# Optimization experiments

Measured on AMD Instinct MI355X. Metric: run time of the kernel, lower is better.

Reference implementation:

```python
import jax, jax.numpy as jnp
import numpy as np
from jax import lax

DN = ('NCHW', 'OIHW', 'NCHW')

def conv2d(x, w, b, pad):
    y = lax.conv_general_dilated(x, w, (1, 1), [(pad, pad), (pad, pad)], dimension_numbers=DN)
    return y + b[None, :, None, None]

def setup_inputs() -> dict:
    key = jax.random.key(0)
    ks = jax.random.split(key, 12)
    B, H, W, C, K = 32, 256, 256, 16, 32
    x = jax.random.normal(ks[0], (B, 1, H, W), jnp.float32)
    s = 0.1
    stem_w = jax.random.normal(ks[1], (C, 1, 3, 3), jnp.float32) * s
    stem_b = jnp.zeros((C,), jnp.float32)
    up1_w = jax.random.normal(ks[2], (C, C, 3, 3), jnp.float32) * s
    up1_b = jnp.zeros((C,), jnp.float32)
    up2_w = jax.random.normal(ks[3], (C, C, 1, 1), jnp.float32) * s
    up2_b = jnp.zeros((C,), jnp.float32)
    tau_w = jax.random.normal(ks[4], (C, C, 1, 1), jnp.float32) * s
    tau_b = jnp.zeros((C,), jnp.float32)
    codebook = jax.random.uniform(ks[5], (K, C), jnp.float32, -1.0 / K, 1.0 / K)
    dec_w = jax.random.normal(ks[6], (1, C, 1, 1), jnp.float32) * s
    dec_b = jnp.zeros((1,), jnp.float32)
    return {"x": x, "stem_w": stem_w, "stem_b": stem_b, "up1_w": up1_w, "up1_b": up1_b,
            "up2_w": up2_w, "up2_b": up2_b, "tau_w": tau_w, "tau_b": tau_b,
            "codebook": codebook, "dec_w": dec_w, "dec_b": dec_b, "n_steps": 5}

def vq(z, codebook):
    # z: [B,C,H,W], codebook: [K,C]
    B, C, H, W = z.shape
    K = codebook.shape[0]
    z_flat = jnp.transpose(z, (0, 2, 3, 1)).reshape(-1, C)  # [N,C]
    dists = (jnp.sum(z_flat ** 2, axis=1, keepdims=True)
             + jnp.sum(codebook ** 2, axis=1)
             - 2.0 * z_flat @ codebook.T)  # [N,K]
    indices = jnp.argmin(dists, axis=1)  # [N]
    z_q = jnp.transpose(codebook[indices].reshape(B, H, W, C), (0, 3, 1, 2))
    commit_loss = jnp.mean((lax.stop_gradient(z_q) - z) ** 2)
    codebook_loss = jnp.mean((z_q - lax.stop_gradient(z)) ** 2)
    vq_loss = codebook_loss + 0.25 * commit_loss
    z_q_st = z + lax.stop_gradient(z_q - z)
    used = jnp.zeros((K,), jnp.float32).at[indices].set(1.0)
    usage = jnp.sum(used) / K
    return z_q_st, vq_loss, usage, indices.reshape(B, H, W)

def reference(x, stem_w, stem_b, up1_w, up1_b, up2_w, up2_b, tau_w, tau_b, codebook, dec_w, dec_b, n_steps):
    state = jax.nn.relu(conv2d(x, stem_w, stem_b, 1))
    vq_total = jnp.float32(0.0)
    usage_total = jnp.float32(0.0)
    for _ in range(n_steps):
        delta = conv2d(jax.nn.relu(conv2d(state, up1_w, up1_b, 1)), up2_w, up2_b, 0)
        beta = jax.nn.sigmoid(conv2d(state, tau_w, tau_b, 0))
        state = beta * state + (1.0 - beta) * delta
        state, vq_loss, usage, _ = vq(state, codebook)
        vq_total = vq_total + vq_loss
        usage_total = usage_total + usage
    output = jax.nn.sigmoid(conv2d(state, dec_w, dec_b, 0))
    return output, vq_total / n_steps, usage_total / n_steps
```

## Files before the change

### kernel.cpp

```cpp
#include <hip/hip_runtime.h>
#include <math.h>

#define DEV __device__ __forceinline__

namespace {
constexpr int B_ = 32, H_ = 256, W_ = 256;
constexpr size_t NPIX = (size_t)B_ * H_ * W_;

constexpr int QT9 = 0;
constexpr int QAB = 5940;
constexpr int QCB = 7220;
constexpr int QU2 = 7860;
constexpr int QTOT = 8116;
constexpr int QLDS = 7220;

constexpr int IW1 = 0;
constexpr int IU2 = 2304;
constexpr int ITA = 2560;
constexpr int ICB = 2816;
constexpr int IB1 = 3456;
constexpr int IB2 = 3472;
constexpr int ITB = 3488;
constexpr int ISB = 3504;
constexpr int ISW = 3520;
constexpr int ITOT = 3664;

constexpr size_t OFF_QTAB = 2 * NPIX;
constexpr size_t OFF_ITAB = OFF_QTAB + (size_t)QTOT * 4;
constexpr size_t OFF_DLUT = OFF_ITAB + (size_t)ITOT * 4;
constexpr size_t OFF_LOSS = (OFF_DLUT + 128 + 7) & ~(size_t)7;
constexpr size_t OFF_MASK = OFF_LOSS + 5 * 8;
}

typedef float f2v __attribute__((ext_vector_type(2)));

struct V16 { f2v h[8]; };

DEV f2v fma2(f2v a, f2v b, f2v c) {
#if __has_builtin(__builtin_elementwise_fma)
    return __builtin_elementwise_fma(a, b, c);
#else
    f2v r; r.x = fmaf(a.x, b.x, c.x); r.y = fmaf(a.y, b.y, c.y); return r;
#endif
}
DEV f2v max2(f2v a, f2v b) {
#if __has_builtin(__builtin_elementwise_max)
    return __builtin_elementwise_max(a, b);
#else
    f2v r; r.x = fmaxf(a.x, b.x); r.y = fmaxf(a.y, b.y); return r;
#endif
}

DEV V16 v16z() {
    V16 r;
    #pragma unroll
    for (int j = 0; j < 8; ++j) r.h[j] = (f2v){0.f, 0.f};
    return r;
}
DEV void v16fma(V16& a, const V16& w, float s) {
    f2v ss = (f2v){s, s};
    #pragma unroll
    for (int j = 0; j < 8; ++j) a.h[j] = fma2(w.h[j], ss, a.h[j]);
}
DEV void v16add(V16& a, const V16& b) {
    #pragma unroll
    for (int j = 0; j < 8; ++j) a.h[j] = a.h[j] + b.h[j];
}
DEV void v16relu(V16& a) {
    f2v z = (f2v){0.f, 0.f};
    #pragma unroll
    for (int j = 0; j < 8; ++j) a.h[j] = max2(a.h[j], z);
}
DEV float v16dot(const V16& a, const V16& b) {
    f2v acc = (f2v){0.f, 0.f};
    #pragma unroll
    for (int j = 0; j < 8; ++j) acc = fma2(a.h[j], b.h[j], acc);
    return acc.x + acc.y;
}
DEV V16 ld16(const float* p) {
    const float4* q = (const float4*)p;
    float4 A = q[0], Bv = q[1], C = q[2], D = q[3];
    V16 r;
    r.h[0] = (f2v){A.x, A.y};  r.h[1] = (f2v){A.z, A.w};
    r.h[2] = (f2v){Bv.x, Bv.y}; r.h[3] = (f2v){Bv.z, Bv.w};
    r.h[4] = (f2v){C.x, C.y};  r.h[5] = (f2v){C.z, C.w};
    r.h[6] = (f2v){D.x, D.y};  r.h[7] = (f2v){D.z, D.w};
    return r;
}
DEV void st16(float* p, const V16& v) {
    float4* q = (float4*)p;
    q[0] = make_float4(v.h[0].x, v.h[0].y, v.h[1].x, v.h[1].y);
    q[1] = make_float4(v.h[2].x, v.h[2].y, v.h[3].x, v.h[3].y);
    q[2] = make_float4(v.h[4].x, v.h[4].y, v.h[5].x, v.h[5].y);
    q[3] = make_float4(v.h[6].x, v.h[6].y, v.h[7].x, v.h[7].y);
}
DEV void v16sig(V16& a) {
    #pragma unroll
    for (int j = 0; j < 8; ++j) {
        a.h[j].x = 1.f / (1.f + expf(-a.h[j].x));
        a.h[j].y = 1.f / (1.f + expf(-a.h[j].y));
    }
}

__global__ void k_setup(const float* __restrict__ w1, const float* __restrict__ b1,
                        const float* __restrict__ u2w, const float* __restrict__ b2,
                        const float* __restrict__ tw, const float* __restrict__ tb,
                        const float* __restrict__ cb, const float* __restrict__ stw,
                        const float* __restrict__ stb, const float* __restrict__ dw,
                        const float* __restrict__ db,
                        float* __restrict__ gQ, float* __restrict__ gI,
                        float* __restrict__ dlut, double* __restrict__ lossS,
                        unsigned int* __restrict__ maskS)
{
    int tid = threadIdx.x;
    if (tid < 5) { lossS[tid] = 0.0; maskS[tid] = 0u; }
    for (int e = tid; e < 297; e += 256) {
        int t = e / 33, k = e % 33;
        float* dst = &gQ[QT9 + e * 20];
        for (int o = 0; o < 16; ++o) {
            float acc = 0.f;
            if (k < 32) {
                for (int i = 0; i < 16; ++i)
                    acc = fmaf(w1[o * 144 + i * 9 + t], cb[k * 16 + i], acc);
                if (t == 4) acc += b1[o];
            }
            dst[o] = acc;
        }
        dst[16] = dst[17] = dst[18] = dst[19] = 0.f;
    }
    if (tid < 32) {
        int k = tid;
        float nrm = 0.f;
        for (int c = 0; c < 16; ++c) { float v = cb[k * 16 + c]; nrm = fmaf(v, v, nrm); }
        for (int c = 0; c < 16; ++c) { gQ[QCB + k * 20 + c] = cb[k * 16 + c]; gI[ICB + k * 20 + c] = cb[k * 16 + c]; }
        gQ[QCB + k * 20 + 16] = nrm; gI[ICB + k * 20 + 16] = nrm;
        for (int c = 17; c < 20; ++c) { gQ[QCB + k * 20 + c] = 0.f; gI[ICB + k * 20 + c] = 0.f; }
        float dacc = db[0];
        for (int c = 0; c < 16; ++c) dacc = fmaf(dw[c], cb[k * 16 + c], dacc);
        dlut[k] = 1.f / (1.f + expf(-dacc));
        for (int c = 0; c < 16; ++c) {
            float ta = tb[c];
            for (int i = 0; i < 16; ++i) ta = fmaf(tw[c * 16 + i], cb[k * 16 + i], ta);
            float beta = 1.f / (1.f + expf(-ta));
            gQ[QAB + k * 20 + c] = beta * cb[k * 16 + c] + (1.f - beta) * b2[c];
            gQ[QAB + (32 + k) * 20 + c] = 1.f - beta;
        }
        for (int c = 16; c < 20; ++c) { gQ[QAB + k * 20 + c] = 0.f; gQ[QAB + (32 + k) * 20 + c] = 0.f; }
    }
    if (tid < 16) {
        int i = tid;
        for (int o = 0; o < 16; ++o) {
            gQ[QU2 + i * 16 + o] = u2w[o * 16 + i];
            gI[IU2 + i * 16 + o] = u2w[o * 16 + i];
            gI[ITA + i * 16 + o] = tw[o * 16 + i];
        }
        gI[IB1 + i] = b1[i]; gI[IB2 + i] = b2[i]; gI[ITB + i] = tb[i]; gI[ISB + i] = stb[i];
    }
    for (int e = tid; e < 144; e += 256) {
        int t = e / 16, i = e % 16;
        float* dst = &gI[IW1 + e * 16];
        for (int o = 0; o < 16; ++o) dst[o] = w1[o * 144 + i * 9 + t];
    }
    if (tid < 9) {
        int t = tid;
        for (int o = 0; o < 16; ++o) gI[ISW + t * 16 + o] = stw[o * 9 + t];
    }
}

__global__ __launch_bounds__(256, 3) void k_iter1(
    const float* __restrict__ x, const float* __restrict__ gI,
    unsigned char* __restrict__ idx_out, double* __restrict__ lossS,
    unsigned int* __restrict__ maskS)
{
    __shared__ __align__(16) float xt[20 * 36];
    __shared__ __align__(16) float stE[306 * 20];
    __shared__ __align__(16) float stO[306 * 20];
    __shared__ double dsum[4];
    __shared__ unsigned int msum[4];
    const int lx = threadIdx.x, ly = threadIdx.y;
    const int lid = ly * 16 + lx;
    const int b = blockIdx.z, oy = blockIdx.y * 16, ox = blockIdx.x * 32;
    const float* xb = x + (size_t)b * (H_ * W_);
    for (int i = lid; i < 720; i += 256) {
        int iy = i / 36, ix = i % 36;
        int gy = oy - 2 + iy, gx = ox - 2 + ix;
        float v = 0.f;
        if ((unsigned)gy < (unsigned)H_ && (unsigned)gx < (unsigned)W_) v = xb[gy * W_ + gx];
        xt[i] = v;
    }
    __syncthreads();
    for (int q = lid; q < 612; q += 256) {
        int sy = q / 34, sx = q % 34;
        int gy = oy - 1 + sy, gx = ox - 1 + sx;
        bool inb = ((unsigned)gy < (unsigned)H_ && (unsigned)gx < (unsigned)W_);
        V16 a = ld16(&gI[ISB]);
        #pragma unroll
        for (int t = 0; t < 9; ++t) {
            float xv = xt[(sy + t / 3) * 36 + sx + t % 3];
            V16 w = ld16(&gI[ISW + t * 16]);
            v16fma(a, w, xv);
        }
        v16relu(a);
        if (!inb) a = v16z();
        float* dst = ((sx & 1) ? stO : stE) + (sy * 17 + (sx >> 1)) * 20;
        st16(dst, a);
    }
    __syncthreads();
    V16 u0 = ld16(&gI[IB1]);
    V16 u1 = u0;
    #pragma unroll
    for (int t = 0; t < 9; ++t) {
        const int r = ly + t / 3, dx = t % 3;
        const float* p0; const float* p1;
        if (dx == 0)      { p0 = &stE[(r * 17 + lx) * 20];     p1 = &stO[(r * 17 + lx) * 20]; }
        else if (dx == 1) { p0 = &stO[(r * 17 + lx) * 20];     p1 = &stE[(r * 17 + lx + 1) * 20]; }
        else              { p0 = &stE[(r * 17 + lx + 1) * 20]; p1 = &stO[(r * 17 + lx + 1) * 20]; }
        V16 s0 = ld16(p0), s1 = ld16(p1);
        const int base = IW1 + t * 256;
        #pragma unroll
        for (int j = 0; j < 8; ++j) {
            f2v a0 = s0.h[j], a1 = s1.h[j];
            V16 wA = ld16(&gI[base + (2 * j) * 16]);
            v16fma(u0, wA, a0.x); v16fma(u1, wA, a1.x);
            V16 wB = ld16(&gI[base + (2 * j + 1) * 16]);
            v16fma(u0, wB, a0.y); v16fma(u1, wB, a1.y);
        }
    }
    v16relu(u0); v16relu(u1);
    V16 c0 = ld16(&stO[((ly + 1) * 17 + lx) * 20]);
    V16 c1 = ld16(&stE[((ly + 1) * 17 + lx + 1) * 20]);
    V16 v0 = ld16(&gI[IB2]);
    V16 v1 = v0;
    #pragma unroll
    for (int j = 0; j < 8; ++j) {
        f2v a0 = u0.h[j], a1 = u1.h[j];
        V16 wA = ld16(&gI[IU2 + (2 * j) * 16]);
        v16fma(v0, wA, a0.x); v16fma(v1, wA, a1.x);
        V16 wB = ld16(&gI[IU2 + (2 * j + 1) * 16]);
        v16fma(v0, wB, a0.y); v16fma(v1, wB, a1.y);
    }
    V16 t0 = ld16(&gI[ITB]);
    V16 t1 = t0;
    #pragma unroll
    for (int j = 0; j < 8; ++j) {
        f2v a0 = c0.h[j], a1 = c1.h[j];
        V16 wA = ld16(&gI[ITA + (2 * j) * 16]);
        v16fma(t0, wA, a0.x); v16fma(t1, wA, a1.x);
        V16 wB = ld16(&gI[ITA + (2 * j + 1) * 16]);
        v16fma(t0, wB, a0.y); v16fma(t1, wB, a1.y);
    }
    v16sig(t0); v16sig(t1);
    V16 z0, z1;
    #pragma unroll
    for (int j = 0; j < 8; ++j) {
        z0.h[j] = fma2(t0.h[j], c0.h[j] - v0.h[j], v0.h[j]);
        z1.h[j] = fma2(t1.h[j], c1.h[j] - v1.h[j], v1.h[j]);
    }
    float zz0 = v16dot(z0, z0), zz1 = v16dot(z1, z1);
    float best0 = 3.4e38f, best1 = 3.4e38f; int bk0 = 0, bk1 = 0;
    #pragma unroll 4
    for (int k = 0; k < 32; ++k) {
        V16 q = ld16(&gI[ICB + k * 20]);
        float cn = gI[ICB + k * 20 + 16];
        float d0 = (zz0 + cn) - 2.0f * v16dot(q, z0);
        float d1 = (zz1 + cn) - 2.0f * v16dot(q, z1);
        if (d0 < best0) { best0 = d0; bk0 = k; }
        if (d1 < best1) { best1 = d1; bk1 = k; }
    }
    unsigned short pr = (unsigned short)(bk0 | (bk1 << 8));
    *(unsigned short*)(idx_out + (size_t)b * (H_ * W_) + (size_t)(oy + ly) * W_ + ox + 2 * lx) = pr;
    float lp = best0 + best1;
    unsigned int m = (1u << bk0) | (1u << bk1);
    #pragma unroll
    for (int off = 32; off > 0; off >>= 1) {
        lp += __shfl_down(lp, off, 64);
        m |= __shfl_down(m, off, 64);
    }
    if ((lid & 63) == 0) { dsum[lid >> 6] = (double)lp; msum[lid >> 6] = m; }
    __syncthreads();
    if (lid == 0) {
        atomicAdd(lossS, dsum[0] + dsum[1] + dsum[2] + dsum[3]);
        atomicOr(maskS, msum[0] | msum[1] | msum[2] | msum[3]);
    }
}

__global__ __launch_bounds__(256, 3) void k_qstep(
    const unsigned char* __restrict__ idx_in, unsigned char* __restrict__ idx_out,
    const float* __restrict__ gQ, double* __restrict__ lossS,
    unsigned int* __restrict__ maskS)
{
    __shared__ __align__(16) float tab[QLDS];
    __shared__ unsigned char ct[18 * 80];
    __shared__ double dsum[4];
    __shared__ unsigned int msum[4];
    const int tx = threadIdx.x, ty = threadIdx.y;
    const int lid = ty * 16 + tx;
    const int b = blockIdx.z, oy = blockIdx.y * 16, ox = blockIdx.x * 64;
    for (int i = lid; i < QLDS / 4; i += 256) ((float4*)tab)[i] = ((const float4*)gQ)[i];
    const unsigned char* ib = idx_in + (size_t)b * (H_ * W_);
    for (int i = lid; i < 18 * 66; i += 256) {
        int r = i / 66, c = i % 66;
        int gy = oy - 1 + r, gx = ox - 1 + c;
        unsigned char v = 32;
        if ((unsigned)gy < (unsigned)H_ && (unsigned)gx < (unsigned)W_) v = ib[gy * W_ + gx];
        ct[r * 80 + c] = v;
    }
    __syncthreads();
    const int cx = tx * 4;
    int K[3][6];
    #pragma unroll
    for (int r = 0; r < 3; ++r) {
        unsigned int w0 = *(const unsigned int*)&ct[(ty + r) * 80 + cx];
        unsigned int w1 = *(const unsigned int*)&ct[(ty + r) * 80 + cx + 4];
        K[r][0] = w0 & 255; K[r][1] = (w0 >> 8) & 255; K[r][2] = (w0 >> 16) & 255;
        K[r][3] = w0 >> 24; K[r][4] = w1 & 255; K[r][5] = (w1 >> 8) & 255;
    }
    V16 V[4];
    #pragma unroll
    for (int half = 0; half < 2; ++half) {
        V16 U0 = v16z(), U1 = v16z();
        const int p0 = half * 2, p1 = half * 2 + 1;
        #pragma unroll
        for (int t = 0; t < 9; ++t) {
            const int dy = t / 3, dx = t % 3;
            V16 e0 = ld16(&tab[(t * 33 + K[dy][p0 + dx]) * 20]);
            v16add(U0, e0);
            V16 e1 = ld16(&tab[(t * 33 + K[dy][p1 + dx]) * 20]);
            v16add(U1, e1);
        }
        v16relu(U0); v16relu(U1);
        V16 v0 = v16z(), v1 = v16z();
        #pragma unroll
        for (int j = 0; j < 8; ++j) {
            f2v a0 = U0.h[j], a1 = U1.h[j];
            V16 wA = ld16(&gQ[QU2 + (2 * j) * 16]);
            v16fma(v0, wA, a0.x); v16fma(v1, wA, a1.x);
            V16 wB = ld16(&gQ[QU2 + (2 * j + 1) * 16]);
            v16fma(v0, wB, a0.y); v16fma(v1, wB, a1.y);
        }
        {
            int kc = K[1][p0 + 1];
            V16 a = ld16(&tab[QAB + kc * 20]);
            V16 bb = ld16(&tab[QAB + (32 + kc) * 20]);
            #pragma unroll
            for (int j = 0; j < 8; ++j) v0.h[j] = fma2(bb.h[j], v0.h[j], a.h[j]);
        }
        {
            int kc = K[1][p1 + 1];
            V16 a = ld16(&tab[QAB + kc * 20]);
            V16 bb = ld16(&tab[QAB + (32 + kc) * 20]);
            #pragma unroll
            for (int j = 0; j < 8; ++j) v1.h[j] = fma2(bb.h[j], v1.h[j], a.h[j]);
        }
        V[p0] = v0; V[p1] = v1;
    }
    float zz[4], best[4]; int bk[4];
    #pragma unroll
    for (int p = 0; p < 4; ++p) { zz[p] = v16dot(V[p], V[p]); best[p] = 3.4e38f; bk[p] = 0; }
    #pragma unroll 4
    for (int k = 0; k < 32; ++k) {
        V16 q = ld16(&gQ[QCB + k * 20]);
        float cn = gQ[QCB + k * 20 + 16];
        #pragma unroll
        for (int p = 0; p < 4; ++p) {
            float d = (zz[p] + cn) - 2.0f * v16dot(q, V[p]);
            if (d < best[p]) { best[p] = d; bk[p] = k; }
        }
    }
    unsigned int pack = (unsigned)bk[0] | ((unsigned)bk[1] << 8) | ((unsigned)bk[2] << 16) | ((unsigned)bk[3] << 24);
    *(unsigned int*)(idx_out + (size_t)b * (H_ * W_) + (size_t)(oy + ty) * W_ + ox + cx) = pack;
    float lp = best[0] + best[1] + best[2] + best[3];
    unsigned int m = (1u << bk[0]) | (1u << bk[1]) | (1u << bk[2]) | (1u << bk[3]);
    #pragma unroll
    for (int off = 32; off > 0; off >>= 1) {
        lp += __shfl_down(lp, off, 64);
        m |= __shfl_down(m, off, 64);
    }
    if ((lid & 63) == 0) { dsum[lid >> 6] = (double)lp; msum[lid >> 6] = m; }
    __syncthreads();
    if (lid == 0) {
        atomicAdd(lossS, dsum[0] + dsum[1] + dsum[2] + dsum[3]);
        atomicOr(maskS, msum[0] | msum[1] | msum[2] | msum[3]);
    }
}

__global__ __launch_bounds__(256) void k_final(
    const unsigned char* __restrict__ idxF, const float* __restrict__ dlut,
    float* __restrict__ out, const double* __restrict__ lossS,
    const unsigned int* __restrict__ maskS)
{
    __shared__ float lut[32];
    if (threadIdx.x < 32) lut[threadIdx.x] = dlut[threadIdx.x];
    __syncthreads();
    size_t i = (size_t)blockIdx.x * 256 + threadIdx.x;
    uchar4 c4 = ((const uchar4*)idxF)[i];
    float4 o4 = make_float4(lut[c4.x], lut[c4.y], lut[c4.z], lut[c4.w]);
    ((float4*)out)[i] = o4;
    if (blockIdx.x == 0 && threadIdx.x == 0) {
        double vq = 0.0; float us = 0.f;
        for (int s = 0; s < 5; ++s) {
            vq += 1.25 * lossS[s] / 33554432.0;
            us += (float)__popc(maskS[s]) / 32.0f;
        }
        out[NPIX] = (float)(vq / 5.0);
        out[NPIX + 1] = us / 5.0f;
    }
}

extern "C" void kernel_launch(void* const* d_in, const int* in_sizes, int n_in,
                              void* d_out, int out_size, void* d_ws, size_t ws_size,
                              hipStream_t stream)
{
    const float* x   = (const float*)d_in[0];
    const float* stw = (const float*)d_in[1];
    const float* stb = (const float*)d_in[2];
    const float* w1  = (const float*)d_in[3];
    const float* b1  = (const float*)d_in[4];
    const float* u2w = (const float*)d_in[5];
    const float* b2  = (const float*)d_in[6];
    const float* tw  = (const float*)d_in[7];
    const float* tb  = (const float*)d_in[8];
    const float* cb  = (const float*)d_in[9];
    const float* dw  = (const float*)d_in[10];
    const float* db  = (const float*)d_in[11];

    char* ws = (char*)d_ws;
    unsigned char* idxA = (unsigned char*)ws;
    unsigned char* idxB = (unsigned char*)(ws + NPIX);
    float* gQ   = (float*)(ws + OFF_QTAB);
    float* gI   = (float*)(ws + OFF_ITAB);
    float* dlut = (float*)(ws + OFF_DLUT);
    double* lossS = (double*)(ws + OFF_LOSS);
    unsigned int* maskS = (unsigned int*)(ws + OFF_MASK);

    dim3 blk(16, 16, 1);
    dim3 g1(W_ / 32, H_ / 16, B_);
    dim3 gq(W_ / 64, H_ / 16, B_);
    k_setup<<<1, 256, 0, stream>>>(w1, b1, u2w, b2, tw, tb, cb, stw, stb, dw, db,
                                   gQ, gI, dlut, lossS, maskS);
    k_iter1<<<g1, blk, 0, stream>>>(x, gI, idxA, lossS + 0, maskS + 0);
    k_qstep<<<gq, blk, 0, stream>>>(idxA, idxB, gQ, lossS + 1, maskS + 1);
    k_qstep<<<gq, blk, 0, stream>>>(idxB, idxA, gQ, lossS + 2, maskS + 2);
    k_qstep<<<gq, blk, 0, stream>>>(idxA, idxB, gQ, lossS + 3, maskS + 3);
    k_qstep<<<gq, blk, 0, stream>>>(idxB, idxA, gQ, lossS + 4, maskS + 4);
    k_final<<<dim3((unsigned)(NPIX / 4 / 256)), 256, 0, stream>>>(idxA, dlut, (float*)d_out, lossS, maskS);
}
```

Baseline: 542.6 us.

## Fuse final decoder LUT into last qstep and interleave VQ search per pixel pair

The last quantization step now writes the decoded float output directly through a 32-entry LUT, removing the separate final kernel's read of the index buffer. Scalar loss and usage finalization moves to a tiny single-block kernel. Inside k_qstep, the codebook argmin runs per half (two pixels) instead of holding four 16-wide vectors, which lowers register pressure, and the launch bound rises to 4 blocks per CU. The iter1 3x3 conv loop is also restructured to load each row's four staged vectors once and reuse them across the three dx taps.

New measurement: 575.4 us. 1.06x slower.

```diff
diff --git a/kernel.cpp b/kernel.cpp
--- a/kernel.cpp
+++ b/kernel.cpp
@@ -209,21 +209,25 @@
     V16 u0 = ld16(&gI[IB1]);
     V16 u1 = u0;
     #pragma unroll
-    for (int t = 0; t < 9; ++t) {
-        const int r = ly + t / 3, dx = t % 3;
-        const float* p0; const float* p1;
-        if (dx == 0)      { p0 = &stE[(r * 17 + lx) * 20];     p1 = &stO[(r * 17 + lx) * 20]; }
-        else if (dx == 1) { p0 = &stO[(r * 17 + lx) * 20];     p1 = &stE[(r * 17 + lx + 1) * 20]; }
-        else              { p0 = &stE[(r * 17 + lx + 1) * 20]; p1 = &stO[(r * 17 + lx + 1) * 20]; }
-        V16 s0 = ld16(p0), s1 = ld16(p1);
-        const int base = IW1 + t * 256;
+    for (int dy = 0; dy < 3; ++dy) {
+        const int r = ly + dy;
+        V16 s0 = ld16(&stE[(r * 17 + lx) * 20]);
+        V16 s1 = ld16(&stO[(r * 17 + lx) * 20]);
+        V16 s2 = ld16(&stE[(r * 17 + lx + 1) * 20]);
+        V16 s3 = ld16(&stO[(r * 17 + lx + 1) * 20]);
         #pragma unroll
-        for (int j = 0; j < 8; ++j) {
-            f2v a0 = s0.h[j], a1 = s1.h[j];
-            V16 wA = ld16(&gI[base + (2 * j) * 16]);
-            v16fma(u0, wA, a0.x); v16fma(u1, wA, a1.x);
-            V16 wB = ld16(&gI[base + (2 * j + 1) * 16]);
-            v16fma(u0, wB, a0.y); v16fma(u1, wB, a1.y);
+        for (int dx = 0; dx < 3; ++dx) {
+            const int base = IW1 + (dy * 3 + dx) * 256;
+            const V16& a0 = (dx == 0) ? s0 : (dx == 1) ? s1 : s2;
+            const V16& a1 = (dx == 0) ? s1 : (dx == 1) ? s2 : s3;
+            #pragma unroll
+            for (int j = 0; j < 8; ++j) {
+                f2v p0 = a0.h[j], p1 = a1.h[j];
+                V16 wA = ld16(&gI[base + (2 * j) * 16]);
+                v16fma(u0, wA, p0.x); v16fma(u1, wA, p1.x);
+                V16 wB = ld16(&gI[base + (2 * j + 1) * 16]);
+                v16fma(u0, wB, p0.y); v16fma(u1, wB, p1.y);
+            }
         }
     }
     v16relu(u0); v16relu(u1);
@@ -284,19 +288,22 @@
     }
 }
 
-__global__ __launch_bounds__(256, 3) void k_qstep(
+__global__ __launch_bounds__(256, 4) void k_qstep(
     const unsigned char* __restrict__ idx_in, unsigned char* __restrict__ idx_out,
     const float* __restrict__ gQ, double* __restrict__ lossS,
-    unsigned int* __restrict__ maskS)
+    unsigned int* __restrict__ maskS, float* __restrict__ out_px,
+    const float* __restrict__ dlut)
 {
     __shared__ __align__(16) float tab[QLDS];
     __shared__ unsigned char ct[18 * 80];
+    __shared__ float lut[32];
     __shared__ double dsum[4];
     __shared__ unsigned int msum[4];
     const int tx = threadIdx.x, ty = threadIdx.y;
     const int lid = ty * 16 + tx;
     const int b = blockIdx.z, oy = blockIdx.y * 16, ox = blockIdx.x * 64;
     for (int i = lid; i < QLDS / 4; i += 256) ((float4*)tab)[i] = ((const float4*)gQ)[i];
+    if (lid < 32) lut[lid] = dlut[lid];
     const unsigned char* ib = idx_in + (size_t)b * (H_ * W_);
     for (int i = lid; i < 18 * 66; i += 256) {
         int r = i / 66, c = i % 66;
@@ -315,11 +322,12 @@
         K[r][0] = w0 & 255; K[r][1] = (w0 >> 8) & 255; K[r][2] = (w0 >> 16) & 255;
         K[r][3] = w0 >> 24; K[r][4] = w1 & 255; K[r][5] = (w1 >> 8) & 255;
     }
-    V16 V[4];
+    int bk[4];
+    float lp = 0.f;
     #pragma unroll
     for (int half = 0; half < 2; ++half) {
+        const int p0 = half * 2, p1 = half * 2 + 1;
         V16 U0 = v16z(), U1 = v16z();
-        const int p0 = half * 2, p1 = half * 2 + 1;
         #pragma unroll
         for (int t = 0; t < 9; ++t) {
             const int dy = t / 3, dx = t % 3;
@@ -352,24 +360,29 @@
             #pragma unroll
             for (int j = 0; j < 8; ++j) v1.h[j] = fma2(bb.h[j], v1.h[j], a.h[j]);
         }
-        V[p0] = v0; V[p1] = v1;
-    }
-    float zz[4], best[4]; int bk[4];
-    #pragma unroll
-    for (int p = 0; p < 4; ++p) { zz[p] = v16dot(V[p], V[p]); best[p] = 3.4e38f; bk[p] = 0; }
-    #pragma unroll 4
-    for (int k = 0; k < 32; ++k) {
-        V16 q = ld16(&gQ[QCB + k * 20]);
-        float cn = gQ[QCB + k * 20 + 16];
-        #pragma unroll
-        for (int p = 0; p < 4; ++p) {
-            float d = (zz[p] + cn) - 2.0f * v16dot(q, V[p]);
-            if (d < best[p]) { best[p] = d; bk[p] = k; }
-        }
-    }
-    unsigned int pack = (unsigned)bk[0] | ((unsigned)bk[1] << 8) | ((unsigned)bk[2] << 16) | ((unsigned)bk[3] << 24);
-    *(unsigned int*)(idx_out + (size_t)b * (H_ * W_) + (size_t)(oy + ty) * W_ + ox + cx) = pack;
-    float lp = best[0] + best[1] + best[2] + best[3];
+        float zz0 = v16dot(v0, v0), zz1 = v16dot(v1, v1);
+        float best0 = 3.4e38f, best1 = 3.4e38f; int b0 = 0, b1 = 0;
+        #pragma unroll 4
+        for (int k = 0; k < 32; ++k) {
+            V16 q = ld16(&gQ[QCB + k * 20]);
+            float cn = gQ[QCB + k * 20 + 16];
+            float d0 = (zz0 + cn) - 2.0f * v16dot(q, v0);
+            float d1 = (zz1 + cn) - 2.0f * v16dot(q, v1);
+            if (d0 < best0) { best0 = d0; b0 = k; }
+            if (d1 < best1) { best1 = d1; b1 = k; }
+        }
+        bk[p0] = b0; bk[p1] = b1;
+        lp += best0 + best1;
+    }
+    const size_t pofs = (size_t)b * (H_ * W_) + (size_t)(oy + ty) * W_ + ox + cx;
+    if (out_px) {
+        float4 o4 = make_float4(lut[bk[0]], lut[bk[1]], lut[bk[2]], lut[bk[3]]);
+        *(float4*)(out_px + pofs) = o4;
+    } else {
+        unsigned int pack = (unsigned)bk[0] | ((unsigned)bk[1] << 8) |
+                            ((unsigned)bk[2] << 16) | ((unsigned)bk[3] << 24);
+        *(unsigned int*)(idx_out + pofs) = pack;
+    }
     unsigned int m = (1u << bk[0]) | (1u << bk[1]) | (1u << bk[2]) | (1u << bk[3]);
     #pragma unroll
     for (int off = 32; off > 0; off >>= 1) {
@@ -384,19 +397,10 @@
     }
 }
 
-__global__ __launch_bounds__(256) void k_final(
-    const unsigned char* __restrict__ idxF, const float* __restrict__ dlut,
-    float* __restrict__ out, const double* __restrict__ lossS,
-    const unsigned int* __restrict__ maskS)
+__global__ void k_scalars(float* __restrict__ out, const double* __restrict__ lossS,
+                          const unsigned int* __restrict__ maskS)
 {
-    __shared__ float lut[32];
-    if (threadIdx.x < 32) lut[threadIdx.x] = dlut[threadIdx.x];
-    __syncthreads();
-    size_t i = (size_t)blockIdx.x * 256 + threadIdx.x;
-    uchar4 c4 = ((const uchar4*)idxF)[i];
-    float4 o4 = make_float4(lut[c4.x], lut[c4.y], lut[c4.z], lut[c4.w]);
-    ((float4*)out)[i] = o4;
-    if (blockIdx.x == 0 && threadIdx.x == 0) {
+    if (threadIdx.x == 0) {
         double vq = 0.0; float us = 0.f;
         for (int s = 0; s < 5; ++s) {
             vq += 1.25 * lossS[s] / 33554432.0;
@@ -436,12 +440,13 @@
     dim3 blk(16, 16, 1);
     dim3 g1(W_ / 32, H_ / 16, B_);
     dim3 gq(W_ / 64, H_ / 16, B_);
+    float* out = (float*)d_out;
     k_setup<<<1, 256, 0, stream>>>(w1, b1, u2w, b2, tw, tb, cb, stw, stb, dw, db,
                                    gQ, gI, dlut, lossS, maskS);
     k_iter1<<<g1, blk, 0, stream>>>(x, gI, idxA, lossS + 0, maskS + 0);
-    k_qstep<<<gq, blk, 0, stream>>>(idxA, idxB, gQ, lossS + 1, maskS + 1);
-    k_qstep<<<gq, blk, 0, stream>>>(idxB, idxA, gQ, lossS + 2, maskS + 2);
-    k_qstep<<<gq, blk, 0, stream>>>(idxA, idxB, gQ, lossS + 3, maskS + 3);
-    k_qstep<<<gq, blk, 0, stream>>>(idxB, idxA, gQ, lossS + 4, maskS + 4);
-    k_final<<<dim3((unsigned)(NPIX / 4 / 256)), 256, 0, stream>>>(idxA, dlut, (float*)d_out, lossS, maskS);
-}
+    k_qstep<<<gq, blk, 0, stream>>>(idxA, idxB, gQ, lossS + 1, maskS + 1, nullptr, dlut);
+    k_qstep<<<gq, blk, 0, stream>>>(idxB, idxA, gQ, lossS + 2, maskS + 2, nullptr, dlut);
+    k_qstep<<<gq, blk, 0, stream>>>(idxA, idxB, gQ, lossS + 3, maskS + 3, nullptr, dlut);
+    k_qstep<<<gq, blk, 0, stream>>>(idxB, idxA, gQ, lossS + 4, maskS + 4, out, dlut);
+    k_scalars<<<1, 64, 0, stream>>>(out, lossS, maskS);
+}
```
